# Kernel tuning notes

Measured on AMD Instinct MI355X. Metric: run time of the kernel, lower is better.

The kernel has to match this reference:

```python
import jax, jax.numpy as jnp
import numpy as np

B, T, C = 4, 2048, 1024
H, DK, DV = 16, 64, 64  # num_heads, qk_length, value_length (must be equal per source bug)


def setup_inputs() -> dict:
    key = jax.random.key(0)
    ks = jax.random.split(key, 11)
    s = 0.02
    return {
        "Q": jax.random.normal(ks[0], (B, T, C), jnp.float32),
        "K": jax.random.normal(ks[1], (B, T, C), jnp.float32),
        "V": jax.random.normal(ks[2], (B, T, C), jnp.float32),
        "Wq": jax.random.normal(ks[3], (C, H * DK), jnp.float32) * s,
        "bq": jnp.zeros((H * DK,), jnp.float32),
        "Wk": jax.random.normal(ks[4], (C, H * DK), jnp.float32) * s,
        "bk": jnp.zeros((H * DK,), jnp.float32),
        "Wv": jax.random.normal(ks[5], (C, H * DK), jnp.float32) * s,
        "bv": jnp.zeros((H * DK,), jnp.float32),
        "Wo": jax.random.normal(ks[6], (H * DV, C), jnp.float32) * s,
        "bo": jnp.zeros((C,), jnp.float32),
    }


def _split_heads(x, d):
    # (B, T, H*d) -> (B, H, T, d)
    b, t, _ = x.shape
    return x.reshape(b, t, H, d).transpose(0, 2, 1, 3)


def reference(Q, K, V, Wq, bq, Wk, bk, Wv, bv, Wo, bo):
    q = _split_heads(Q @ Wq + bq, DK)  # (B,H,T,DK)
    k = _split_heads(K @ Wk + bk, DK)
    v = _split_heads(V @ Wv + bv, DV)
    scores = jnp.einsum("bhqd,bhkd->bhqk", q, k) / jnp.sqrt(jnp.float32(DK))
    weights = jax.nn.softmax(scores, axis=-1)  # materialized (B,H,T,T) as in source
    attn = jnp.einsum("bhqk,bhkd->bhqd", weights, v)  # (B,H,T,DV)
    # Faithful to source combine_heads: raw view (B,H,T,DV) -> (B,T,H*DV) WITHOUT transposing
    out = attn.reshape(B, T, H * DV)
    return out @ Wo + bo
```

## Files before the change

### kernel.cpp

```cpp
#include <hip/hip_runtime.h>

typedef unsigned short u16;
typedef __attribute__((ext_vector_type(8))) short bf16x8;
typedef __attribute__((ext_vector_type(4))) float f32x4;

__device__ __forceinline__ u16 f2bf(float f) {
  union { float fv; unsigned u; } v; v.fv = f;
  unsigned r = v.u + 0x7fffu + ((v.u >> 16) & 1u);
  return (u16)(r >> 16);
}

__device__ __forceinline__ void gload_lds16(const void* g, void* l) {
  __builtin_amdgcn_global_load_lds(
      (const __attribute__((address_space(1))) unsigned*)g,
      (__attribute__((address_space(3))) unsigned*)l, 16, 0, 0);
}

__device__ __forceinline__ int swz128(int o) { return o ^ ((o >> 3) & 0x70); }

__global__ __launch_bounds__(256) void cvt_bf16_kernel(const float* __restrict__ x,
                                                       u16* __restrict__ y) {
  const int i = (blockIdx.x * 256 + threadIdx.x) * 4;
  const float4 v = *(const float4*)(x + i);
  ushort4 o;
  o.x = f2bf(v.x); o.y = f2bf(v.y); o.z = f2bf(v.z); o.w = f2bf(v.w);
  *(ushort4*)(y + i) = o;
}

__global__ __launch_bounds__(256) void transpose_cvt_kernel(const float* __restrict__ W,
                                                            u16* __restrict__ WT) {
  __shared__ float tile[32][33];
  const int bx = blockIdx.x * 32, by = blockIdx.y * 32;
  const int tx = threadIdx.x, ty = threadIdx.y;
  #pragma unroll
  for (int i = 0; i < 32; i += 8)
    tile[ty + i][tx] = W[(size_t)(by + ty + i) * 1024 + bx + tx];
  __syncthreads();
  #pragma unroll
  for (int i = 0; i < 32; i += 8)
    WT[(size_t)(bx + ty + i) * 1024 + by + tx] = f2bf(tile[tx][ty + i]);
}

template <int MODE>
__global__ __launch_bounds__(256) void gemm128_kernel(
    const u16* __restrict__ A, const u16* __restrict__ BT,
    const float* __restrict__ bias, void* __restrict__ out) {
  __shared__ u16 As[128 * 32];
  __shared__ u16 Bs[128 * 32];
  const int tid = threadIdx.x;
  const int w = tid >> 6, lane = tid & 63;
  const int wr = w >> 1, wc = w & 1;
  const int l16 = lane & 15, lhi = lane >> 4;
  const int lg = (blockIdx.x & 7) * 64 + (blockIdx.x >> 3);
  const int m0 = (lg >> 3) * 128, n0 = (lg & 7) * 128;

  f32x4 acc[4][4] = {};

  for (int kt = 0; kt < 32; ++kt) {
    #pragma unroll
    for (int i = 0; i < 2; ++i) {
      const int ob = w * 2048 + i * 1024;
      const int o = ob + (lane << 4);
      const int row = o >> 6, kbyte = o & 63;
      gload_lds16((const char*)A + (((size_t)(m0 + row)) << 11) + (kt << 6) + kbyte,
                  (char*)As + ob);
      gload_lds16((const char*)BT + (((size_t)(n0 + row)) << 11) + (kt << 6) + kbyte,
                  (char*)Bs + ob);
    }
    __syncthreads();
    bf16x8 a[4], b[4];
    #pragma unroll
    for (int i = 0; i < 4; ++i)
      a[i] = *(const bf16x8*)(As + (wr * 64 + i * 16 + l16) * 32 + lhi * 8);
    #pragma unroll
    for (int j = 0; j < 4; ++j)
      b[j] = *(const bf16x8*)(Bs + (wc * 64 + j * 16 + l16) * 32 + lhi * 8);
    #pragma unroll
    for (int i = 0; i < 4; ++i)
      #pragma unroll
      for (int j = 0; j < 4; ++j)
        acc[i][j] = __builtin_amdgcn_mfma_f32_16x16x32_bf16(a[i], b[j], acc[i][j], 0, 0, 0);
    __syncthreads();
  }

  #pragma unroll
  for (int i = 0; i < 4; ++i) {
    #pragma unroll
    for (int j = 0; j < 4; ++j) {
      const int n = n0 + wc * 64 + j * 16 + l16;
      const float bn = bias[n];
      #pragma unroll
      for (int r = 0; r < 4; ++r) {
        const int m = m0 + wr * 64 + i * 16 + lhi * 4 + r;
        float v = acc[i][j][r] + bn;
        const int bb = m >> 11, t = m & 2047, h = n >> 6, d = n & 63;
        if constexpr (MODE == 0) {
          v *= 0.18033688f;
          ((u16*)out)[((((size_t)bb * 16 + h) * 2048 + t) << 6) + d] = f2bf(v);
        } else if constexpr (MODE == 1) {
          ((u16*)out)[((((size_t)bb * 16 + h) * 2048 + t) << 6) + d] = f2bf(v);
        } else if constexpr (MODE == 2) {
          ((u16*)out)[(((size_t)bb * 16 + h) * 64 + d) * 2048 + t] = f2bf(v);
        } else {
          ((float*)out)[(size_t)m * 1024 + n] = v;
        }
      }
    }
  }
}

__global__ __launch_bounds__(512) void attn_kernel(
    const u16* __restrict__ qh, const u16* __restrict__ kh,
    const u16* __restrict__ vth, u16* __restrict__ outPre) {
  __shared__ u16 Kbuf[2][64 * 64];
  __shared__ u16 Vbuf[64 * 64];
  __shared__ u16 Pl[8][16 * 64];

  const int tid = threadIdx.x, w = tid >> 6, lane = tid & 63;
  const int l16 = lane & 15, lhi = lane >> 4;

  const int wg = (blockIdx.x & 7) * 128 + (blockIdx.x >> 3);
  const int qt = wg & 15, hb = wg >> 4;
  const int h = hb & 15, b = hb >> 4;

  const size_t bh = (size_t)b * 16 + h;
  const u16* qb = qh + bh * (2048 * 64);
  const u16* kb = kh + bh * (2048 * 64);
  const u16* vb = vth + bh * (64 * 2048);

  const int qr0 = qt * 128 + w * 16;
  bf16x8 aq[2];
  #pragma unroll
  for (int c = 0; c < 2; ++c)
    aq[c] = *(const bf16x8*)(qb + (qr0 + l16) * 64 + c * 32 + lhi * 8);

  bf16x8 ones;
  #pragma unroll
  for (int e = 0; e < 8; ++e) ones[e] = (short)0x3F80;

  f32x4 acc_o[4] = {};
  f32x4 acc_l = {};

  auto stageK = [&](int buf, int kv) {
    char* Kt = (char*)&Kbuf[buf][0];
    const int ob = w * 1024;
    const int os = swz128(ob + (lane << 4));
    gload_lds16((const char*)kb + ((size_t)kv << 7) + os, Kt + ob);
  };
  auto stageV = [&](int kv) {
    char* Vt = (char*)&Vbuf[0];
    const int ob = w * 1024;
    const int os = swz128(ob + (lane << 4));
    const int dd = os >> 7, j0 = (os & 127) >> 1;
    gload_lds16((const char*)vb + ((size_t)dd << 12) + (((size_t)(kv + j0)) << 1),
                Vt + ob);
  };

  stageK(0, 0);

  for (int t = 0; t < 32; ++t) {
    const int buf = t & 1;
    __syncthreads();
    stageV(t * 64);

    const char* Kt = (const char*)&Kbuf[buf][0];

    f32x4 s[4];
    #pragma unroll
    for (int jt = 0; jt < 4; ++jt) s[jt] = f32x4{-4.f, -4.f, -4.f, -4.f};
    __builtin_amdgcn_s_setprio(1);
    #pragma unroll
    for (int c = 0; c < 2; ++c) {
      #pragma unroll
      for (int jt = 0; jt < 4; ++jt) {
        const bf16x8 bk = *(const bf16x8*)(Kt +
            swz128((jt * 16 + l16) * 128 + c * 64 + lhi * 16));
        s[jt] = __builtin_amdgcn_mfma_f32_16x16x32_bf16(aq[c], bk, s[jt], 0, 0, 0);
      }
    }
    __builtin_amdgcn_s_setprio(0);

    #pragma unroll
    for (int jt = 0; jt < 4; ++jt)
      #pragma unroll
      for (int r = 0; r < 4; ++r)
        s[jt][r] = __builtin_amdgcn_exp2f(s[jt][r]);

    char* Pw = (char*)&Pl[w][0];
    #pragma unroll
    for (int jt = 0; jt < 4; ++jt)
      #pragma unroll
      for (int r = 0; r < 4; ++r) {
        union { float f; unsigned u; } pv;
        pv.f = s[jt][r];
        *(u16*)(Pw + swz128((lhi * 4 + r) * 128 + (jt * 16 + l16) * 2)) =
            (u16)((pv.u + 0x8000u) >> 16);
      }

    __syncthreads();
    if (t < 31) stageK(buf ^ 1, (t + 1) * 64);

    const char* Vt = (const char*)&Vbuf[0];

    __builtin_amdgcn_s_setprio(1);
    #pragma unroll
    for (int c = 0; c < 2; ++c) {
      const bf16x8 ap = *(const bf16x8*)(Pw +
          swz128(l16 * 128 + c * 64 + lhi * 16));
      acc_l = __builtin_amdgcn_mfma_f32_16x16x32_bf16(ap, ones, acc_l, 0, 0, 0);
      #pragma unroll
      for (int dt = 0; dt < 4; ++dt) {
        const bf16x8 bv = *(const bf16x8*)(Vt +
            swz128((dt * 16 + l16) * 128 + c * 64 + lhi * 16));
        acc_o[dt] = __builtin_amdgcn_mfma_f32_16x16x32_bf16(ap, bv, acc_o[dt], 0, 0, 0);
      }
    }
    __builtin_amdgcn_s_setprio(0);
  }

  #pragma unroll
  for (int dt = 0; dt < 4; ++dt) {
    #pragma unroll
    for (int r = 0; r < 4; ++r) {
      const int t = qr0 + lhi * 4 + r;
      const int d = dt * 16 + l16;
      const float v = acc_o[dt][r] / acc_l[r];
      const int rr = h * 128 + (t >> 4);
      const int cc = ((t & 15) << 6) + d;
      outPre[((size_t)b * 2048 + rr) * 1024 + cc] = f2bf(v);
    }
  }
}

extern "C" void kernel_launch(void* const* d_in, const int* in_sizes, int n_in,
                              void* d_out, int out_size, void* d_ws, size_t ws_size,
                              hipStream_t stream) {
  const float* Q  = (const float*)d_in[0];
  const float* K  = (const float*)d_in[1];
  const float* V  = (const float*)d_in[2];
  const float* Wq = (const float*)d_in[3];
  const float* bq = (const float*)d_in[4];
  const float* Wk = (const float*)d_in[5];
  const float* bk = (const float*)d_in[6];
  const float* Wv = (const float*)d_in[7];
  const float* bv = (const float*)d_in[8];
  const float* Wo = (const float*)d_in[9];
  const float* bo = (const float*)d_in[10];

  char* ws = (char*)d_ws;
  const size_t ACT = 16777216;
  u16* act = (u16*)(ws);
  u16* qhd = (u16*)(ws + ACT);
  u16* khd = (u16*)(ws + 2 * ACT);
  u16* vtd = (u16*)(ws + 3 * ACT);
  u16* wt  = (u16*)(ws + 4 * ACT);

  const dim3 tb(32, 8), tg(32, 32);
  const int cvtBlocks = 8388608 / 4 / 256;

  transpose_cvt_kernel<<<tg, tb, 0, stream>>>(Wq, wt);
  cvt_bf16_kernel<<<cvtBlocks, 256, 0, stream>>>(Q, act);
  gemm128_kernel<0><<<512, 256, 0, stream>>>(act, wt, bq, qhd);
  transpose_cvt_kernel<<<tg, tb, 0, stream>>>(Wk, wt);
  cvt_bf16_kernel<<<cvtBlocks, 256, 0, stream>>>(K, act);
  gemm128_kernel<1><<<512, 256, 0, stream>>>(act, wt, bk, khd);
  transpose_cvt_kernel<<<tg, tb, 0, stream>>>(Wv, wt);
  cvt_bf16_kernel<<<cvtBlocks, 256, 0, stream>>>(V, act);
  gemm128_kernel<2><<<512, 256, 0, stream>>>(act, wt, bv, vtd);
  attn_kernel<<<1024, 512, 0, stream>>>(qhd, khd, vtd, act);
  transpose_cvt_kernel<<<tg, tb, 0, stream>>>(Wo, wt);
  gemm128_kernel<3><<<512, 256, 0, stream>>>(act, wt, bo, (float*)d_out);
}
```

Baseline: 246.9 us.

## Fuse fp32-to-bf16 conversion into a single batched QKV projection GEMM

Removes the separate activation conversion kernels. The new projection GEMM reads fp32 Q/K/V directly, converts to bf16 in registers and stores to LDS. The three projections run in one 1536-block launch, and all four weight transposes are batched into one launch. This cuts launch count and the round trip of bf16 activations through global memory, but A-tile loads become synchronous register loads rather than direct-to-LDS loads, and each tile now reads twice the bytes.

```diff
diff --git a/kernel.cpp b/kernel.cpp
--- a/kernel.cpp
+++ b/kernel.cpp
@@ -10,6 +10,12 @@
   return (u16)(r >> 16);
 }
 
+__device__ __forceinline__ unsigned pkbf(float a, float b) {
+  union { float f; unsigned u; } ua, ub;
+  ua.f = a; ub.f = b;
+  return ((ub.u + 0x8000u) & 0xFFFF0000u) | ((ua.u + 0x8000u) >> 16);
+}
+
 __device__ __forceinline__ void gload_lds16(const void* g, void* l) {
   __builtin_amdgcn_global_load_lds(
       (const __attribute__((address_space(1))) unsigned*)g,
@@ -18,18 +24,15 @@
 
 __device__ __forceinline__ int swz128(int o) { return o ^ ((o >> 3) & 0x70); }
 
-__global__ __launch_bounds__(256) void cvt_bf16_kernel(const float* __restrict__ x,
-                                                       u16* __restrict__ y) {
-  const int i = (blockIdx.x * 256 + threadIdx.x) * 4;
-  const float4 v = *(const float4*)(x + i);
-  ushort4 o;
-  o.x = f2bf(v.x); o.y = f2bf(v.y); o.z = f2bf(v.z); o.w = f2bf(v.w);
-  *(ushort4*)(y + i) = o;
-}
-
-__global__ __launch_bounds__(256) void transpose_cvt_kernel(const float* __restrict__ W,
-                                                            u16* __restrict__ WT) {
+__global__ __launch_bounds__(256) void transpose_cvt4_kernel(
+    const float* __restrict__ W0, const float* __restrict__ W1,
+    const float* __restrict__ W2, const float* __restrict__ W3,
+    u16* __restrict__ T0, u16* __restrict__ T1,
+    u16* __restrict__ T2, u16* __restrict__ T3) {
   __shared__ float tile[32][33];
+  const int z = blockIdx.z;
+  const float* W = z == 0 ? W0 : z == 1 ? W1 : z == 2 ? W2 : W3;
+  u16* WT = z == 0 ? T0 : z == 1 ? T1 : z == 2 ? T2 : T3;
   const int bx = blockIdx.x * 32, by = blockIdx.y * 32;
   const int tx = threadIdx.x, ty = threadIdx.y;
   #pragma unroll
@@ -41,10 +44,94 @@
     WT[(size_t)(bx + ty + i) * 1024 + by + tx] = f2bf(tile[tx][ty + i]);
 }
 
-template <int MODE>
-__global__ __launch_bounds__(256) void gemm128_kernel(
+__global__ __launch_bounds__(256) void proj_gemm_kernel(
+    const float* __restrict__ Qf, const float* __restrict__ Kf,
+    const float* __restrict__ Vf,
+    const u16* __restrict__ WTq, const u16* __restrict__ WTk,
+    const u16* __restrict__ WTv,
+    const float* __restrict__ bqp, const float* __restrict__ bkp,
+    const float* __restrict__ bvp,
+    u16* __restrict__ qhd, u16* __restrict__ khd, u16* __restrict__ vtd) {
+  __shared__ u16 As[128 * 32];
+  __shared__ u16 Bs[128 * 32];
+  const int tid = threadIdx.x;
+  const int w = tid >> 6, lane = tid & 63;
+  const int wr = w >> 1, wc = w & 1;
+  const int l16 = lane & 15, lhi = lane >> 4;
+  const int lg = (blockIdx.x & 7) * 192 + (blockIdx.x >> 3);
+  const int proj = lg >> 9, inner = lg & 511;
+  const int m0 = (inner >> 3) * 128, n0 = (inner & 7) * 128;
+  const float* A  = proj == 0 ? Qf : proj == 1 ? Kf : Vf;
+  const u16*   BT = proj == 0 ? WTq : proj == 1 ? WTk : WTv;
+  const float* bias = proj == 0 ? bqp : proj == 1 ? bkp : bvp;
+
+  const int arow = tid >> 2, ac = (tid & 3) * 8;
+
+  f32x4 acc[4][4] = {};
+
+  for (int kt = 0; kt < 32; ++kt) {
+    #pragma unroll
+    for (int i = 0; i < 2; ++i) {
+      const int ob = w * 2048 + i * 1024;
+      const int o = ob + (lane << 4);
+      const int row = o >> 6, kbyte = o & 63;
+      gload_lds16((const char*)BT + (((size_t)(n0 + row)) << 11) + (kt << 6) + kbyte,
+                  (char*)Bs + ob);
+    }
+    #pragma unroll
+    for (int i = 0; i < 2; ++i) {
+      const int r = arow + i * 64;
+      const float* ap = A + (size_t)(m0 + r) * 1024 + kt * 32 + ac;
+      const float4 v0 = *(const float4*)(ap);
+      const float4 v1 = *(const float4*)(ap + 4);
+      uint4 pk;
+      pk.x = pkbf(v0.x, v0.y); pk.y = pkbf(v0.z, v0.w);
+      pk.z = pkbf(v1.x, v1.y); pk.w = pkbf(v1.z, v1.w);
+      *(uint4*)((char*)As + r * 64 + ac * 2) = pk;
+    }
+    __syncthreads();
+    bf16x8 a[4], b[4];
+    #pragma unroll
+    for (int i = 0; i < 4; ++i)
+      a[i] = *(const bf16x8*)(As + (wr * 64 + i * 16 + l16) * 32 + lhi * 8);
+    #pragma unroll
+    for (int j = 0; j < 4; ++j)
+      b[j] = *(const bf16x8*)(Bs + (wc * 64 + j * 16 + l16) * 32 + lhi * 8);
+    #pragma unroll
+    for (int i = 0; i < 4; ++i)
+      #pragma unroll
+      for (int j = 0; j < 4; ++j)
+        acc[i][j] = __builtin_amdgcn_mfma_f32_16x16x32_bf16(a[i], b[j], acc[i][j], 0, 0, 0);
+    __syncthreads();
+  }
+
+  #pragma unroll
+  for (int i = 0; i < 4; ++i) {
+    #pragma unroll
+    for (int j = 0; j < 4; ++j) {
+      const int n = (inner & 7) * 128 + wc * 64 + j * 16 + l16;
+      const float bn = bias[n];
+      #pragma unroll
+      for (int r = 0; r < 4; ++r) {
+        const int m = m0 + wr * 64 + i * 16 + lhi * 4 + r;
+        float v = acc[i][j][r] + bn;
+        const int bb = m >> 11, t = m & 2047, h = n >> 6, d = n & 63;
+        if (proj == 0) {
+          v *= 0.18033688f;
+          qhd[((((size_t)bb * 16 + h) * 2048 + t) << 6) + d] = f2bf(v);
+        } else if (proj == 1) {
+          khd[((((size_t)bb * 16 + h) * 2048 + t) << 6) + d] = f2bf(v);
+        } else {
+          vtd[(((size_t)bb * 16 + h) * 64 + d) * 2048 + t] = f2bf(v);
+        }
+      }
+    }
+  }
+}
+
+__global__ __launch_bounds__(256) void out_gemm_kernel(
     const u16* __restrict__ A, const u16* __restrict__ BT,
-    const float* __restrict__ bias, void* __restrict__ out) {
+    const float* __restrict__ bias, float* __restrict__ out) {
   __shared__ u16 As[128 * 32];
   __shared__ u16 Bs[128 * 32];
   const int tid = threadIdx.x;
@@ -92,18 +179,7 @@
       #pragma unroll
       for (int r = 0; r < 4; ++r) {
         const int m = m0 + wr * 64 + i * 16 + lhi * 4 + r;
-        float v = acc[i][j][r] + bn;
-        const int bb = m >> 11, t = m & 2047, h = n >> 6, d = n & 63;
-        if constexpr (MODE == 0) {
-          v *= 0.18033688f;
-          ((u16*)out)[((((size_t)bb * 16 + h) * 2048 + t) << 6) + d] = f2bf(v);
-        } else if constexpr (MODE == 1) {
-          ((u16*)out)[((((size_t)bb * 16 + h) * 2048 + t) << 6) + d] = f2bf(v);
-        } else if constexpr (MODE == 2) {
-          ((u16*)out)[(((size_t)bb * 16 + h) * 64 + d) * 2048 + t] = f2bf(v);
-        } else {
-          ((float*)out)[(size_t)m * 1024 + n] = v;
-        }
+        out[(size_t)m * 1024 + n] = acc[i][j][r] + bn;
       }
     }
   }
@@ -253,21 +329,15 @@
   u16* qhd = (u16*)(ws + ACT);
   u16* khd = (u16*)(ws + 2 * ACT);
   u16* vtd = (u16*)(ws + 3 * ACT);
-  u16* wt  = (u16*)(ws + 4 * ACT);
-
-  const dim3 tb(32, 8), tg(32, 32);
-  const int cvtBlocks = 8388608 / 4 / 256;
-
-  transpose_cvt_kernel<<<tg, tb, 0, stream>>>(Wq, wt);
-  cvt_bf16_kernel<<<cvtBlocks, 256, 0, stream>>>(Q, act);
-  gemm128_kernel<0><<<512, 256, 0, stream>>>(act, wt, bq, qhd);
-  transpose_cvt_kernel<<<tg, tb, 0, stream>>>(Wk, wt);
-  cvt_bf16_kernel<<<cvtBlocks, 256, 0, stream>>>(K, act);
-  gemm128_kernel<1><<<512, 256, 0, stream>>>(act, wt, bk, khd);
-  transpose_cvt_kernel<<<tg, tb, 0, stream>>>(Wv, wt);
-  cvt_bf16_kernel<<<cvtBlocks, 256, 0, stream>>>(V, act);
-  gemm128_kernel<2><<<512, 256, 0, stream>>>(act, wt, bv, vtd);
+  u16* wtq = (u16*)(ws);
+  u16* wtk = (u16*)(ws + 2097152);
+  u16* wtv = (u16*)(ws + 2 * 2097152);
+  u16* wto = (u16*)(ws + 4 * ACT);
+
+  transpose_cvt4_kernel<<<dim3(32, 32, 4), dim3(32, 8), 0, stream>>>(
+      Wq, Wk, Wv, Wo, wtq, wtk, wtv, wto);
+  proj_gemm_kernel<<<1536, 256, 0, stream>>>(Q, K, V, wtq, wtk, wtv,
+                                             bq, bk, bv, qhd, khd, vtd);
   attn_kernel<<<1024, 512, 0, stream>>>(qhd, khd, vtd, act);
-  transpose_cvt_kernel<<<tg, tb, 0, stream>>>(Wo, wt);
-  gemm128_kernel<3><<<512, 256, 0, stream>>>(act, wt, bo, (float*)d_out);
-}
+  out_gemm_kernel<<<512, 256, 0, stream>>>(act, wto, bo, (float*)d_out);
+}
```

After: 240.3 us. 1.03x faster.

## Swizzle GEMM LDS tiles and batch all weight transposes into one launch

Applied to the files above, without the earlier changes.

The GEMM now applies an XOR swizzle to the LDS tile layout. The swizzle is applied to the global source addresses of the direct-to-LDS loads and to the matching MFMA operand reads, with the aim of reducing LDS bank conflicts on the 64-byte-row tiles. The four separate weight transpose/convert launches are merged into one launch with a z-dimension selecting the matrix, writing into four separate workspace buffers. This removes three kernel launches, at the cost of extra workspace.

```diff
diff --git a/kernel.cpp b/kernel.cpp
--- a/kernel.cpp
+++ b/kernel.cpp
@@ -17,6 +17,7 @@
 }
 
 __device__ __forceinline__ int swz128(int o) { return o ^ ((o >> 3) & 0x70); }
+__device__ __forceinline__ int swz64(int o) { return o ^ (((o >> 7) & 3) << 4); }
 
 __global__ __launch_bounds__(256) void cvt_bf16_kernel(const float* __restrict__ x,
                                                        u16* __restrict__ y) {
@@ -27,9 +28,15 @@
   *(ushort4*)(y + i) = o;
 }
 
-__global__ __launch_bounds__(256) void transpose_cvt_kernel(const float* __restrict__ W,
-                                                            u16* __restrict__ WT) {
+__global__ __launch_bounds__(256) void transpose_cvt4_kernel(
+    const float* __restrict__ W0, const float* __restrict__ W1,
+    const float* __restrict__ W2, const float* __restrict__ W3,
+    u16* __restrict__ T0, u16* __restrict__ T1,
+    u16* __restrict__ T2, u16* __restrict__ T3) {
   __shared__ float tile[32][33];
+  const int z = blockIdx.z;
+  const float* W = z == 0 ? W0 : z == 1 ? W1 : z == 2 ? W2 : W3;
+  u16* WT = z == 0 ? T0 : z == 1 ? T1 : z == 2 ? T2 : T3;
   const int bx = blockIdx.x * 32, by = blockIdx.y * 32;
   const int tx = threadIdx.x, ty = threadIdx.y;
   #pragma unroll
@@ -60,21 +67,23 @@
     #pragma unroll
     for (int i = 0; i < 2; ++i) {
       const int ob = w * 2048 + i * 1024;
-      const int o = ob + (lane << 4);
-      const int row = o >> 6, kbyte = o & 63;
-      gload_lds16((const char*)A + (((size_t)(m0 + row)) << 11) + (kt << 6) + kbyte,
+      const int os = swz64(ob + (lane << 4));
+      const int row = os >> 6, kb = os & 63;
+      gload_lds16((const char*)A + (((size_t)(m0 + row)) << 11) + (kt << 6) + kb,
                   (char*)As + ob);
-      gload_lds16((const char*)BT + (((size_t)(n0 + row)) << 11) + (kt << 6) + kbyte,
+      gload_lds16((const char*)BT + (((size_t)(n0 + row)) << 11) + (kt << 6) + kb,
                   (char*)Bs + ob);
     }
     __syncthreads();
     bf16x8 a[4], b[4];
     #pragma unroll
     for (int i = 0; i < 4; ++i)
-      a[i] = *(const bf16x8*)(As + (wr * 64 + i * 16 + l16) * 32 + lhi * 8);
+      a[i] = *(const bf16x8*)((const char*)As +
+             swz64((wr * 64 + i * 16 + l16) * 64 + lhi * 16));
     #pragma unroll
     for (int j = 0; j < 4; ++j)
-      b[j] = *(const bf16x8*)(Bs + (wc * 64 + j * 16 + l16) * 32 + lhi * 8);
+      b[j] = *(const bf16x8*)((const char*)Bs +
+             swz64((wc * 64 + j * 16 + l16) * 64 + lhi * 16));
     #pragma unroll
     for (int i = 0; i < 4; ++i)
       #pragma unroll
@@ -249,25 +258,26 @@
 
   char* ws = (char*)d_ws;
   const size_t ACT = 16777216;
+  u16* abf = (u16*)(ws);
   u16* act = (u16*)(ws);
   u16* qhd = (u16*)(ws + ACT);
   u16* khd = (u16*)(ws + 2 * ACT);
   u16* vtd = (u16*)(ws + 3 * ACT);
-  u16* wt  = (u16*)(ws + 4 * ACT);
-
-  const dim3 tb(32, 8), tg(32, 32);
+  u16* wtq = (u16*)(ws + 4 * ACT);
+  u16* wtk = (u16*)(ws + 4 * ACT + 2097152);
+  u16* wtv = (u16*)(ws + 4 * ACT + 2 * 2097152);
+  u16* wto = (u16*)(ws + 4 * ACT + 3 * 2097152);
+
   const int cvtBlocks = 8388608 / 4 / 256;
 
-  transpose_cvt_kernel<<<tg, tb, 0, stream>>>(Wq, wt);
-  cvt_bf16_kernel<<<cvtBlocks, 256, 0, stream>>>(Q, act);
-  gemm128_kernel<0><<<512, 256, 0, stream>>>(act, wt, bq, qhd);
-  transpose_cvt_kernel<<<tg, tb, 0, stream>>>(Wk, wt);
-  cvt_bf16_kernel<<<cvtBlocks, 256, 0, stream>>>(K, act);
-  gemm128_kernel<1><<<512, 256, 0, stream>>>(act, wt, bk, khd);
-  transpose_cvt_kernel<<<tg, tb, 0, stream>>>(Wv, wt);
-  cvt_bf16_kernel<<<cvtBlocks, 256, 0, stream>>>(V, act);
-  gemm128_kernel<2><<<512, 256, 0, stream>>>(act, wt, bv, vtd);
+  transpose_cvt4_kernel<<<dim3(32, 32, 4), dim3(32, 8), 0, stream>>>(
+      Wq, Wk, Wv, Wo, wtq, wtk, wtv, wto);
+  cvt_bf16_kernel<<<cvtBlocks, 256, 0, stream>>>(Q, abf);
+  gemm128_kernel<0><<<512, 256, 0, stream>>>(abf, wtq, bq, qhd);
+  cvt_bf16_kernel<<<cvtBlocks, 256, 0, stream>>>(K, abf);
+  gemm128_kernel<1><<<512, 256, 0, stream>>>(abf, wtk, bk, khd);
+  cvt_bf16_kernel<<<cvtBlocks, 256, 0, stream>>>(V, abf);
+  gemm128_kernel<2><<<512, 256, 0, stream>>>(abf, wtv, bv, vtd);
   attn_kernel<<<1024, 512, 0, stream>>>(qhd, khd, vtd, act);
-  transpose_cvt_kernel<<<tg, tb, 0, stream>>>(Wo, wt);
-  gemm128_kernel<3><<<512, 256, 0, stream>>>(act, wt, bo, (float*)d_out);
-}
+  gemm128_kernel<3><<<512, 256, 0, stream>>>(act, wto, bo, (float*)d_out);
+}
```

New measurement: 232.5 us. 5.8% less time.
